# Optimization experiments

Hardware: AMD Instinct MI355X
Metric: run time of the kernel (lower is better)

Reference implementation:

```python
import jax, jax.numpy as jnp
import numpy as np

L = 2          # num_bigbird_encoder_blocks
H = 8          # n_heads
BS = 64        # block_size
G = 2          # num_global_blocks
W = 3          # window_size (blocks)
EPS = 1e-8


def rmsnorm(x, w, eps=EPS):
    return x * jax.lax.rsqrt(jnp.mean(x * x, axis=-1, keepdims=True) + eps) * w


def setup_inputs() -> dict:
    key = jax.random.key(0)
    ks = jax.random.split(key, 12)
    B, S, D, F, V = 8, 2048, 256, 1024, 32000
    nB = S // BS
    inp = {
        "input_ids": jax.random.randint(ks[0], (B, S), 0, V, dtype=jnp.int64),
        "rand_idx": jax.random.randint(ks[1], (nB, 2), 0, nB, dtype=jnp.int32),
        "emb": jax.random.normal(ks[2], (V, D), jnp.float32) * 0.02,
        "ln1_w": jnp.ones((L, D), jnp.float32),
        "wq": jax.random.normal(ks[3], (L, D, D), jnp.float32) / np.sqrt(D),
        "wk": jax.random.normal(ks[4], (L, D, D), jnp.float32) / np.sqrt(D),
        "wv": jax.random.normal(ks[5], (L, D, D), jnp.float32) / np.sqrt(D),
        "wo": jax.random.normal(ks[6], (L, D, D), jnp.float32) / np.sqrt(D),
        "ln2_w": jnp.ones((L, D), jnp.float32),
        "w1": jax.random.normal(ks[7], (L, D, F), jnp.float32) / np.sqrt(D),
        "w2": jax.random.normal(ks[8], (L, F, D), jnp.float32) / np.sqrt(F),
        "final_ln_w": jnp.ones((D,), jnp.float32),
    }
    return inp


def _split_heads(x, B, nB, dh):
    # [B,S,D] -> [B,H,nB,bs,dh]
    return x.reshape(B, nB, BS, H, dh).transpose(0, 3, 1, 2, 4)


def reference(input_ids, rand_idx, emb, ln1_w, wq, wk, wv, wo, ln2_w, w1, w2, final_ln_w):
    B, S = input_ids.shape
    D = emb.shape[1]
    dh = D // H
    nB = S // BS
    scale = 1.0 / np.sqrt(dh)

    # block-sparse key-block indices per query block: global + sliding window + random
    blocks = jnp.arange(nB)
    win = jnp.clip(blocks[:, None] + jnp.arange(-(W // 2), W // 2 + 1)[None, :], 0, nB - 1)
    glob = jnp.broadcast_to(jnp.arange(G), (nB, G))
    idx = jnp.concatenate([glob, win, rand_idx.astype(jnp.int32)], axis=1)  # [nB, M], M=7
    M = idx.shape[1]

    x = emb[input_ids]  # [B,S,D]
    for l in range(L):
        h = rmsnorm(x, ln1_w[l])
        q = _split_heads(h @ wq[l], B, nB, dh)  # [B,H,nB,bs,dh]
        k = _split_heads(h @ wk[l], B, nB, dh)
        v = _split_heads(h @ wv[l], B, nB, dh)
        k_sel = k[:, :, idx]  # [B,H,nB,M,bs,dh]
        v_sel = v[:, :, idx]
        scores = jnp.einsum("bhnqd,bhnmsd->bhnqms", q, k_sel) * scale
        a = jax.nn.softmax(scores.reshape(B, H, nB, BS, M * BS), axis=-1)
        a = a.reshape(B, H, nB, BS, M, BS)
        o = jnp.einsum("bhnqms,bhnmsd->bhnqd", a, v_sel)
        o = o.transpose(0, 2, 3, 1, 4).reshape(B, S, D)
        x = x + o @ wo[l]
        h2 = rmsnorm(x, ln2_w[l])
        x = x + jax.nn.gelu(h2 @ w1[l]) @ w2[l]
    return rmsnorm(x, final_ln_w)
```

## Files before the change

kernel.cpp:

```cpp
#include <hip/hip_runtime.h>
#include <cstdint>
#include <cstddef>

typedef __bf16 bf16x8 __attribute__((ext_vector_type(8)));
typedef __bf16 bf16x4 __attribute__((ext_vector_type(4)));
typedef float  f32x4  __attribute__((ext_vector_type(4)));
typedef unsigned u32x2 __attribute__((ext_vector_type(2)));
typedef unsigned u32x4 __attribute__((ext_vector_type(4)));

#define DMODEL 256

__device__ __forceinline__ float bflo(unsigned u) { return __builtin_bit_cast(float, u << 16); }
__device__ __forceinline__ float bfhi(unsigned u) { return __builtin_bit_cast(float, u & 0xffff0000u); }
__device__ __forceinline__ unsigned short bfbits(float f) {
  return __builtin_bit_cast(unsigned short, (__bf16)f);
}

#define GLOAD_LDS16(gp, lp) __builtin_amdgcn_global_load_lds(                 \
    (const __attribute__((address_space(1))) unsigned*)(gp),                  \
    (__attribute__((address_space(3))) unsigned*)(lp), 16, 0, 0)

__global__ void transpose_all(const float* __restrict__ wq, const float* __restrict__ wk,
                              const float* __restrict__ wv, const float* __restrict__ wo,
                              const float* __restrict__ w1, const float* __restrict__ w2,
                              __bf16* __restrict__ wbase) {
  int idx = blockIdx.x * 256 + threadIdx.x;
  int l = idx >= 786432;
  int r = idx - l * 786432;
  __bf16* wb = wbase + (size_t)l * 786432;
  const float* s; __bf16* d; int R, C, e;
  if (r < 65536)       { s = wq + l * 65536;  d = wb;          R = 256;  C = 256;  e = r; }
  else if (r < 131072) { s = wk + l * 65536;  d = wb + 65536;  R = 256;  C = 256;  e = r - 65536; }
  else if (r < 196608) { s = wv + l * 65536;  d = wb + 131072; R = 256;  C = 256;  e = r - 131072; }
  else if (r < 262144) { s = wo + l * 65536;  d = wb + 196608; R = 256;  C = 256;  e = r - 196608; }
  else if (r < 524288) { s = w1 + l * 262144; d = wb + 262144; R = 256;  C = 1024; e = r - 262144; }
  else                 { s = w2 + l * 262144; d = wb + 524288; R = 1024; C = 256;  e = r - 524288; }
  int row = e / C, col = e - row * C;
  d[col * R + row] = (__bf16)s[e];
}

__global__ void embed_k(const int* __restrict__ ids, const float* __restrict__ emb, float* __restrict__ x) {
  int row = blockIdx.x * 4 + (threadIdx.x >> 6);
  int lane = threadIdx.x & 63;
  int id = ids[row];
  ((f32x4*)(x + (size_t)row * DMODEL))[lane] = ((const f32x4*)(emb + (size_t)id * DMODEL))[lane];
}

template<typename OUT>
__global__ void rmsnorm_k(const float* __restrict__ x, const float* __restrict__ w, OUT* __restrict__ out) {
  int row = blockIdx.x * 4 + (threadIdx.x >> 6);
  int lane = threadIdx.x & 63;
  f32x4 v = ((const f32x4*)(x + (size_t)row * DMODEL))[lane];
  float ss = v[0]*v[0] + v[1]*v[1] + v[2]*v[2] + v[3]*v[3];
  #pragma unroll
  for (int off = 1; off < 64; off <<= 1) ss += __shfl_xor(ss, off);
  float rms = rsqrtf(ss * (1.0f / DMODEL) + 1e-8f);
  f32x4 wv = ((const f32x4*)w)[lane];
  if constexpr (sizeof(OUT) == 4) {
    f32x4 o;
    o[0] = v[0]*rms*wv[0]; o[1] = v[1]*rms*wv[1]; o[2] = v[2]*rms*wv[2]; o[3] = v[3]*rms*wv[3];
    ((f32x4*)((float*)out + (size_t)row * DMODEL))[lane] = o;
  } else {
    bf16x4 o;
    o[0] = (__bf16)(v[0]*rms*wv[0]); o[1] = (__bf16)(v[1]*rms*wv[1]);
    o[2] = (__bf16)(v[2]*rms*wv[2]); o[3] = (__bf16)(v[3]*rms*wv[3]);
    ((bf16x4*)((__bf16*)out + (size_t)row * DMODEL))[lane] = o;
  }
}

__device__ __forceinline__ float gelu_f(float v) {
  return 0.5f * v * (1.0f + tanhf(0.7978845608028654f * (v + 0.044715f * v * v * v)));
}

template<bool RES, bool GELU, bool OUTB>
__launch_bounds__(256)
__global__ void gemm_bt(const __bf16* __restrict__ A, const __bf16* __restrict__ Bt,
                        __bf16* __restrict__ outb, float* __restrict__ res,
                        int K, int N) {
  __shared__ char sm[32768];
  int tid = threadIdx.x;
  int lane = tid & 63;
  int w = tid >> 6;
  int wr = w >> 1, wc = w & 1;
  int lr = lane & 15;
  int hk = lane >> 4;
  size_t bm = (size_t)blockIdx.x * 128, bn = (size_t)blockIdx.y * 128;
  const __bf16* Ab = A + bm * (size_t)K;
  const __bf16* Bb = Bt + bn * (size_t)K;

  int u0 = w * 128 + lane;
  int r0 = u0 >> 2, c0 = u0 & 3;
  int u1 = u0 + 64;
  int r1 = u1 >> 2, c1 = u1 & 3;
  size_t ga0 = (size_t)r0 * K + c0 * 8;
  size_t ga1 = (size_t)r1 * K + c1 * 8;
  int lb0 = (w * 2) * 1024;
  int lb1 = (w * 2 + 1) * 1024;

  int nt = K >> 5;
  GLOAD_LDS16(Ab + ga0, sm + lb0);
  GLOAD_LDS16(Bb + ga0, sm + 8192 + lb0);
  GLOAD_LDS16(Ab + ga1, sm + lb1);
  GLOAD_LDS16(Bb + ga1, sm + 8192 + lb1);
  __syncthreads();

  f32x4 acc[4][4] = {};
  for (int t = 0; t < nt; ++t) {
    char* cur = sm + (t & 1) * 16384;
    if (t + 1 < nt) {
      char* nxt = sm + ((t + 1) & 1) * 16384;
      int kk = (t + 1) * 32;
      GLOAD_LDS16(Ab + ga0 + kk, nxt + lb0);
      GLOAD_LDS16(Bb + ga0 + kk, nxt + 8192 + lb0);
      GLOAD_LDS16(Ab + ga1 + kk, nxt + lb1);
      GLOAD_LDS16(Bb + ga1 + kk, nxt + 8192 + lb1);
    }
    bf16x8 av[4], bv[4];
    #pragma unroll
    for (int i = 0; i < 4; ++i)
      av[i] = *(const bf16x8*)(cur + (wr * 64 + i * 16 + lr) * 64 + hk * 16);
    #pragma unroll
    for (int i = 0; i < 4; ++i)
      bv[i] = *(const bf16x8*)(cur + 8192 + (wc * 64 + i * 16 + lr) * 64 + hk * 16);
    #pragma unroll
    for (int mi = 0; mi < 4; ++mi)
      #pragma unroll
      for (int ni = 0; ni < 4; ++ni)
        acc[mi][ni] = __builtin_amdgcn_mfma_f32_16x16x32_bf16(av[mi], bv[ni], acc[mi][ni], 0, 0, 0);
    __syncthreads();
  }

  size_t row0 = bm + wr * 64 + (hk << 2);
  size_t col0 = bn + wc * 64 + lr;
  #pragma unroll
  for (int mi = 0; mi < 4; ++mi)
    #pragma unroll
    for (int ni = 0; ni < 4; ++ni)
      #pragma unroll
      for (int j = 0; j < 4; ++j) {
        size_t row = row0 + mi * 16 + j, col = col0 + ni * 16;
        float val = acc[mi][ni][j];
        if constexpr (GELU) val = gelu_f(val);
        if constexpr (RES)  res[row * N + col] += val;
        if constexpr (OUTB) outb[row * N + col] = (__bf16)val;
      }
}

#define ATTN_LDS 28672

__launch_bounds__(256, 3)
__global__ void attn_k(const __bf16* __restrict__ qkv, const int* __restrict__ rand_idx,
                       __bf16* __restrict__ o) {
  extern __shared__ char smKV[];
  int tid = threadIdx.x;
  int lane = tid & 63;
  int w = tid >> 6;
  int q16 = lane & 15, g = lane >> 4;

  int bid = blockIdx.x;
  int b = bid >> 8;
  int hh = (bid >> 5) & 7;
  int n = bid & 31;
  int r5 = rand_idx[n * 2], r6 = rand_idx[n * 2 + 1];
  int nm1 = n > 0 ? n - 1 : 0;
  int np1 = n < 31 ? n + 1 : 31;
  size_t base = (size_t)b * 2048;

  #pragma unroll
  for (int it = 0; it < 7; ++it) {
    int chunk = it * 256 + tid;
    int r = chunk >> 2, c16 = chunk & 3;
    int m = r >> 6, si = r & 63;
    int kb = m == 0 ? 0 : m == 1 ? 1 : m == 2 ? nm1 : m == 3 ? n : m == 4 ? np1 : m == 5 ? r5 : r6;
    u32x4 d = *(const u32x4*)(qkv + (base + kb * 64 + si) * 768 + 256 + hh * 32 + c16 * 8);
    *(u32x4*)(smKV + ((chunk * 16) ^ ((r & 7) << 4))) = d;
  }

  bf16x8 qf = *(const bf16x8*)(qkv + (base + n * 64 + w * 16 + q16) * 768 + hh * 32 + g * 8);

  __syncthreads();

  f32x4 st[28];
  __builtin_amdgcn_s_setprio(1);
  #pragma unroll
  for (int t = 0; t < 28; ++t) {
    int row = 16 * t + q16;
    bf16x8 kf = *(const bf16x8*)(smKV + ((row * 64 + g * 16) ^ ((q16 & 7) << 4)));
    st[t] = __builtin_amdgcn_mfma_f32_16x16x32_bf16(kf, qf, (f32x4){0.f, 0.f, 0.f, 0.f}, 0, 0, 0);
  }
  __builtin_amdgcn_s_setprio(0);

  float m0 = st[0][0], m1 = st[0][1], m2 = st[0][2], m3 = st[0][3];
  #pragma unroll
  for (int t = 1; t < 28; ++t) {
    m0 = fmaxf(m0, st[t][0]); m1 = fmaxf(m1, st[t][1]);
    m2 = fmaxf(m2, st[t][2]); m3 = fmaxf(m3, st[t][3]);
  }
  float mx = fmaxf(fmaxf(m0, m1), fmaxf(m2, m3));
  mx = fmaxf(mx, __shfl_xor(mx, 16));
  mx = fmaxf(mx, __shfl_xor(mx, 32));
  const float SC = 0.17677669529663687f * 1.4426950408889634f;
  float mc = mx * SC;

  unsigned pk0[28], pk1[28];
  float ssum = 0.f;
  #pragma unroll
  for (int t = 0; t < 28; ++t) {
    float e0 = __builtin_amdgcn_exp2f(fmaf(st[t][0], SC, -mc));
    float e1 = __builtin_amdgcn_exp2f(fmaf(st[t][1], SC, -mc));
    float e2 = __builtin_amdgcn_exp2f(fmaf(st[t][2], SC, -mc));
    float e3 = __builtin_amdgcn_exp2f(fmaf(st[t][3], SC, -mc));
    ssum += (e0 + e1) + (e2 + e3);
    pk0[t] = (unsigned)bfbits(e0) | ((unsigned)bfbits(e1) << 16);
    pk1[t] = (unsigned)bfbits(e2) | ((unsigned)bfbits(e3) << 16);
  }
  ssum += __shfl_xor(ssum, 16);
  ssum += __shfl_xor(ssum, 32);
  float inv = 1.0f / ssum;

  unsigned vreg[4][8];
  #pragma unroll
  for (int it = 0; it < 4; ++it) {
    int item = it * 256 + tid;
    if (item < 896) {
      int dp = item & 15, ko = item >> 4;
      int s0 = ko * 8;
      int m = s0 >> 6, si = s0 & 63;
      int kb = m == 0 ? 0 : m == 1 ? 1 : m == 2 ? nm1 : m == 3 ? n : m == 4 ? np1 : m == 5 ? r5 : r6;
      const unsigned* vs = (const unsigned*)(qkv + (base + kb * 64 + si) * 768 + 512 + hh * 32) + dp;
      #pragma unroll
      for (int i = 0; i < 8; ++i) vreg[it][i] = vs[(size_t)i * 384];
    }
  }

  __syncthreads();

  #pragma unroll
  for (int it = 0; it < 4; ++it) {
    int item = it * 256 + tid;
    if (item < 896) {
      int dp = item & 15, ko = item >> 4;
      u32x4 lo4, hi4;
      #pragma unroll
      for (int wd = 0; wd < 4; ++wd) {
        unsigned a = vreg[it][2 * wd], bb = vreg[it][2 * wd + 1];
        lo4[wd] = (a & 0xffffu) | (bb << 16);
        hi4[wd] = (a >> 16) | (bb & 0xffff0000u);
      }
      unsigned swz = (unsigned)((dp & 7) << 4);
      int byte0 = (2 * dp) * 896 + ko * 16;
      *(u32x4*)(smKV + (byte0 ^ swz)) = lo4;
      *(u32x4*)(smKV + ((byte0 + 896) ^ swz)) = hi4;
    }
  }

  __syncthreads();

  int src0 = q16 + 32 * (g & 1);
  int src1 = src0 + 16;
  bool hi = (g >= 2);
  f32x4 oacc[2] = {};
  __builtin_amdgcn_s_setprio(1);
  #pragma unroll
  for (int ks = 0; ks < 14; ++ks) {
    unsigned a0 = __shfl(pk0[2 * ks], src0), b0 = __shfl(pk0[2 * ks + 1], src0);
    unsigned a1 = __shfl(pk1[2 * ks], src0), b1 = __shfl(pk1[2 * ks + 1], src0);
    unsigned a2 = __shfl(pk0[2 * ks], src1), b2 = __shfl(pk0[2 * ks + 1], src1);
    unsigned a3 = __shfl(pk1[2 * ks], src1), b3 = __shfl(pk1[2 * ks + 1], src1);
    u32x4 pw;
    pw[0] = hi ? b0 : a0; pw[1] = hi ? b1 : a1;
    pw[2] = hi ? b2 : a2; pw[3] = hi ? b3 : a3;
    bf16x8 pf = __builtin_bit_cast(bf16x8, pw);
    #pragma unroll
    for (int dt = 0; dt < 2; ++dt) {
      int d = 16 * dt + q16;
      bf16x8 vf = *(const bf16x8*)(smKV + ((d * 896 + 64 * ks + 16 * g) ^ (((d >> 1) & 7) << 4)));
      oacc[dt] = __builtin_amdgcn_mfma_f32_16x16x32_bf16(vf, pf, oacc[dt], 0, 0, 0);
    }
  }
  __builtin_amdgcn_s_setprio(0);

  size_t orow = (base + n * 64 + w * 16 + q16) * 256 + hh * 32;
  #pragma unroll
  for (int dt = 0; dt < 2; ++dt) {
    u32x2 pk;
    pk[0] = (unsigned)bfbits(oacc[dt][0] * inv) | ((unsigned)bfbits(oacc[dt][1] * inv) << 16);
    pk[1] = (unsigned)bfbits(oacc[dt][2] * inv) | ((unsigned)bfbits(oacc[dt][3] * inv) << 16);
    *(u32x2*)(o + orow + 16 * dt + 4 * g) = pk;
  }
}

extern "C" void kernel_launch(void* const* d_in, const int* in_sizes, int n_in,
                              void* d_out, int out_size, void* d_ws, size_t ws_size,
                              hipStream_t stream) {
  const int*   ids      = (const int*)d_in[0];
  const int*   rand_idx = (const int*)d_in[1];
  const float* emb      = (const float*)d_in[2];
  const float* ln1      = (const float*)d_in[3];
  const float* wq       = (const float*)d_in[4];
  const float* wk       = (const float*)d_in[5];
  const float* wv       = (const float*)d_in[6];
  const float* wo       = (const float*)d_in[7];
  const float* ln2      = (const float*)d_in[8];
  const float* w1       = (const float*)d_in[9];
  const float* w2       = (const float*)d_in[10];
  const float* fln      = (const float*)d_in[11];
  float* out = (float*)d_out;

  char* ws = (char*)d_ws;
  float*  x    = (float*)ws;
  __bf16* h    = (__bf16*)(ws + 16777216);
  __bf16* qkv  = (__bf16*)(ws + 25165824);
  __bf16* obuf = (__bf16*)(ws + 50331648);
  __bf16* g    = qkv;
  __bf16* wbase = (__bf16*)(ws + 58720256);

  transpose_all<<<6144, 256, 0, stream>>>(wq, wk, wv, wo, w1, w2, wbase);
  embed_k<<<4096, 256, 0, stream>>>(ids, emb, x);

  for (int l = 0; l < 2; ++l) {
    __bf16* qkvT = wbase + (size_t)l * 786432;
    __bf16* woT  = qkvT + 196608;
    __bf16* w1T  = woT + 65536;
    __bf16* w2T  = w1T + 262144;

    rmsnorm_k<__bf16><<<4096, 256, 0, stream>>>(x, ln1 + (size_t)l * 256, h);
    gemm_bt<false, false, true><<<dim3(128, 6), 256, 0, stream>>>(h, qkvT, qkv, nullptr, 256, 768);
    attn_k<<<2048, 256, ATTN_LDS, stream>>>(qkv, rand_idx, obuf);
    gemm_bt<true, false, false><<<dim3(128, 2), 256, 0, stream>>>(obuf, woT, nullptr, x, 256, 256);
    rmsnorm_k<__bf16><<<4096, 256, 0, stream>>>(x, ln2 + (size_t)l * 256, h);
    gemm_bt<false, true, true><<<dim3(128, 8), 256, 0, stream>>>(h, w1T, g, nullptr, 256, 1024);
    gemm_bt<true, false, false><<<dim3(128, 2), 256, 0, stream>>>(g, w2T, nullptr, x, 1024, 256);
  }

  rmsnorm_k<float><<<4096, 256, 0, stream>>>(x, fln, out);
}
```

Measured before the change: 408.5 us.

## Restructure block-sparse attention as chunked online softmax with separate V LDS

The attention kernel now loads K and transposed V into separate LDS regions up front. It replaces the full 28-tile score materialization with a 7-chunk online-softmax loop that uses a lazy rescale threshold. The block index is also remapped so that consecutive workgroups span different batches. This is meant to cut register pressure (no 56 packed probability registers and no staged V registers) and to remove the extra barrier between phases. In exchange it doubles LDS per block, drops the occupancy hint, and adds per-chunk reductions and shuffles.

```diff
diff --git a/kernel.cpp b/kernel.cpp
--- a/kernel.cpp
+++ b/kernel.cpp
@@ -146,18 +146,20 @@
       }
 }
 
-#define ATTN_LDS 28672
-
-__launch_bounds__(256, 3)
+#define ATTN_LDS 57344
+
+__launch_bounds__(256)
 __global__ void attn_k(const __bf16* __restrict__ qkv, const int* __restrict__ rand_idx,
                        __bf16* __restrict__ o) {
-  extern __shared__ char smKV[];
+  extern __shared__ char sm[];
+  char* smVt = sm + 28672;
   int tid = threadIdx.x;
   int lane = tid & 63;
   int w = tid >> 6;
   int q16 = lane & 15, g = lane >> 4;
 
-  int bid = blockIdx.x;
+  int bid0 = blockIdx.x;
+  int bid = (bid0 & 7) * 256 + (bid0 >> 3);
   int b = bid >> 8;
   int hh = (bid >> 5) & 7;
   int n = bid & 31;
@@ -173,52 +175,9 @@
     int m = r >> 6, si = r & 63;
     int kb = m == 0 ? 0 : m == 1 ? 1 : m == 2 ? nm1 : m == 3 ? n : m == 4 ? np1 : m == 5 ? r5 : r6;
     u32x4 d = *(const u32x4*)(qkv + (base + kb * 64 + si) * 768 + 256 + hh * 32 + c16 * 8);
-    *(u32x4*)(smKV + ((chunk * 16) ^ ((r & 7) << 4))) = d;
-  }
-
-  bf16x8 qf = *(const bf16x8*)(qkv + (base + n * 64 + w * 16 + q16) * 768 + hh * 32 + g * 8);
-
-  __syncthreads();
-
-  f32x4 st[28];
-  __builtin_amdgcn_s_setprio(1);
-  #pragma unroll
-  for (int t = 0; t < 28; ++t) {
-    int row = 16 * t + q16;
-    bf16x8 kf = *(const bf16x8*)(smKV + ((row * 64 + g * 16) ^ ((q16 & 7) << 4)));
-    st[t] = __builtin_amdgcn_mfma_f32_16x16x32_bf16(kf, qf, (f32x4){0.f, 0.f, 0.f, 0.f}, 0, 0, 0);
-  }
-  __builtin_amdgcn_s_setprio(0);
-
-  float m0 = st[0][0], m1 = st[0][1], m2 = st[0][2], m3 = st[0][3];
-  #pragma unroll
-  for (int t = 1; t < 28; ++t) {
-    m0 = fmaxf(m0, st[t][0]); m1 = fmaxf(m1, st[t][1]);
-    m2 = fmaxf(m2, st[t][2]); m3 = fmaxf(m3, st[t][3]);
-  }
-  float mx = fmaxf(fmaxf(m0, m1), fmaxf(m2, m3));
-  mx = fmaxf(mx, __shfl_xor(mx, 16));
-  mx = fmaxf(mx, __shfl_xor(mx, 32));
-  const float SC = 0.17677669529663687f * 1.4426950408889634f;
-  float mc = mx * SC;
-
-  unsigned pk0[28], pk1[28];
-  float ssum = 0.f;
-  #pragma unroll
-  for (int t = 0; t < 28; ++t) {
-    float e0 = __builtin_amdgcn_exp2f(fmaf(st[t][0], SC, -mc));
-    float e1 = __builtin_amdgcn_exp2f(fmaf(st[t][1], SC, -mc));
-    float e2 = __builtin_amdgcn_exp2f(fmaf(st[t][2], SC, -mc));
-    float e3 = __builtin_amdgcn_exp2f(fmaf(st[t][3], SC, -mc));
-    ssum += (e0 + e1) + (e2 + e3);
-    pk0[t] = (unsigned)bfbits(e0) | ((unsigned)bfbits(e1) << 16);
-    pk1[t] = (unsigned)bfbits(e2) | ((unsigned)bfbits(e3) << 16);
-  }
-  ssum += __shfl_xor(ssum, 16);
-  ssum += __shfl_xor(ssum, 32);
-  float inv = 1.0f / ssum;
-
-  unsigned vreg[4][8];
+    *(u32x4*)(sm + ((chunk * 16) ^ ((r & 7) << 4))) = d;
+  }
+
   #pragma unroll
   for (int it = 0; it < 4; ++it) {
     int item = it * 256 + tid;
@@ -228,58 +187,99 @@
       int m = s0 >> 6, si = s0 & 63;
       int kb = m == 0 ? 0 : m == 1 ? 1 : m == 2 ? nm1 : m == 3 ? n : m == 4 ? np1 : m == 5 ? r5 : r6;
       const unsigned* vs = (const unsigned*)(qkv + (base + kb * 64 + si) * 768 + 512 + hh * 32) + dp;
-      #pragma unroll
-      for (int i = 0; i < 8; ++i) vreg[it][i] = vs[(size_t)i * 384];
-    }
-  }
-
-  __syncthreads();
-
-  #pragma unroll
-  for (int it = 0; it < 4; ++it) {
-    int item = it * 256 + tid;
-    if (item < 896) {
-      int dp = item & 15, ko = item >> 4;
+      unsigned vr[8];
+      #pragma unroll
+      for (int i = 0; i < 8; ++i) vr[i] = vs[(size_t)i * 384];
       u32x4 lo4, hi4;
       #pragma unroll
       for (int wd = 0; wd < 4; ++wd) {
-        unsigned a = vreg[it][2 * wd], bb = vreg[it][2 * wd + 1];
+        unsigned a = vr[2 * wd], bb = vr[2 * wd + 1];
         lo4[wd] = (a & 0xffffu) | (bb << 16);
         hi4[wd] = (a >> 16) | (bb & 0xffff0000u);
       }
       unsigned swz = (unsigned)((dp & 7) << 4);
       int byte0 = (2 * dp) * 896 + ko * 16;
-      *(u32x4*)(smKV + (byte0 ^ swz)) = lo4;
-      *(u32x4*)(smKV + ((byte0 + 896) ^ swz)) = hi4;
-    }
-  }
+      *(u32x4*)(smVt + (byte0 ^ swz)) = lo4;
+      *(u32x4*)(smVt + ((byte0 + 896) ^ swz)) = hi4;
+    }
+  }
+
+  bf16x8 qf = *(const bf16x8*)(qkv + (base + n * 64 + w * 16 + q16) * 768 + hh * 32 + g * 8);
 
   __syncthreads();
 
+  const float SC  = 0.17677669529663687f * 1.4426950408889634f;
+  const float THR = 8.0f / SC;
   int src0 = q16 + 32 * (g & 1);
   int src1 = src0 + 16;
   bool hi = (g >= 2);
+  float m_run = -1e30f, mc = 0.f, ssum = 0.f;
   f32x4 oacc[2] = {};
-  __builtin_amdgcn_s_setprio(1);
-  #pragma unroll
-  for (int ks = 0; ks < 14; ++ks) {
-    unsigned a0 = __shfl(pk0[2 * ks], src0), b0 = __shfl(pk0[2 * ks + 1], src0);
-    unsigned a1 = __shfl(pk1[2 * ks], src0), b1 = __shfl(pk1[2 * ks + 1], src0);
-    unsigned a2 = __shfl(pk0[2 * ks], src1), b2 = __shfl(pk0[2 * ks + 1], src1);
-    unsigned a3 = __shfl(pk1[2 * ks], src1), b3 = __shfl(pk1[2 * ks + 1], src1);
-    u32x4 pw;
-    pw[0] = hi ? b0 : a0; pw[1] = hi ? b1 : a1;
-    pw[2] = hi ? b2 : a2; pw[3] = hi ? b3 : a3;
-    bf16x8 pf = __builtin_bit_cast(bf16x8, pw);
-    #pragma unroll
-    for (int dt = 0; dt < 2; ++dt) {
-      int d = 16 * dt + q16;
-      bf16x8 vf = *(const bf16x8*)(smKV + ((d * 896 + 64 * ks + 16 * g) ^ (((d >> 1) & 7) << 4)));
-      oacc[dt] = __builtin_amdgcn_mfma_f32_16x16x32_bf16(vf, pf, oacc[dt], 0, 0, 0);
-    }
-  }
-  __builtin_amdgcn_s_setprio(0);
-
+  bool first = true;
+
+  #pragma unroll
+  for (int c = 0; c < 7; ++c) {
+    f32x4 st[4];
+    #pragma unroll
+    for (int tl = 0; tl < 4; ++tl) {
+      int row = 16 * (4 * c + tl) + q16;
+      bf16x8 kf = *(const bf16x8*)(sm + ((row * 64 + g * 16) ^ ((q16 & 7) << 4)));
+      st[tl] = __builtin_amdgcn_mfma_f32_16x16x32_bf16(kf, qf, (f32x4){0.f, 0.f, 0.f, 0.f}, 0, 0, 0);
+    }
+    float lm = st[0][0];
+    #pragma unroll
+    for (int tl = 0; tl < 4; ++tl) {
+      lm = fmaxf(lm, fmaxf(fmaxf(st[tl][0], st[tl][1]), fmaxf(st[tl][2], st[tl][3])));
+    }
+    lm = fmaxf(lm, __shfl_xor(lm, 16));
+    lm = fmaxf(lm, __shfl_xor(lm, 32));
+    if (first || !__all(lm <= m_run + THR)) {
+      float nm = fmaxf(m_run, lm);
+      float sf = __builtin_amdgcn_exp2f((m_run - nm) * SC);
+      ssum *= sf;
+      #pragma unroll
+      for (int dt = 0; dt < 2; ++dt)
+        #pragma unroll
+        for (int j = 0; j < 4; ++j) oacc[dt][j] *= sf;
+      m_run = nm;
+      mc = nm * SC;
+      first = false;
+    }
+    unsigned pk0[4], pk1[4];
+    #pragma unroll
+    for (int tl = 0; tl < 4; ++tl) {
+      float e0 = __builtin_amdgcn_exp2f(fmaf(st[tl][0], SC, -mc));
+      float e1 = __builtin_amdgcn_exp2f(fmaf(st[tl][1], SC, -mc));
+      float e2 = __builtin_amdgcn_exp2f(fmaf(st[tl][2], SC, -mc));
+      float e3 = __builtin_amdgcn_exp2f(fmaf(st[tl][3], SC, -mc));
+      ssum += (e0 + e1) + (e2 + e3);
+      pk0[tl] = (unsigned)bfbits(e0) | ((unsigned)bfbits(e1) << 16);
+      pk1[tl] = (unsigned)bfbits(e2) | ((unsigned)bfbits(e3) << 16);
+    }
+    #pragma unroll
+    for (int ksl = 0; ksl < 2; ++ksl) {
+      int ks = 2 * c + ksl;
+      int lt0 = 2 * ksl, lt1 = 2 * ksl + 1;
+      unsigned a0 = __shfl(pk0[lt0], src0), b0 = __shfl(pk0[lt1], src0);
+      unsigned a1 = __shfl(pk1[lt0], src0), b1 = __shfl(pk1[lt1], src0);
+      unsigned a2 = __shfl(pk0[lt0], src1), b2 = __shfl(pk0[lt1], src1);
+      unsigned a3 = __shfl(pk1[lt0], src1), b3 = __shfl(pk1[lt1], src1);
+      u32x4 pw;
+      pw[0] = hi ? b0 : a0; pw[1] = hi ? b1 : a1;
+      pw[2] = hi ? b2 : a2; pw[3] = hi ? b3 : a3;
+      bf16x8 pf = __builtin_bit_cast(bf16x8, pw);
+      #pragma unroll
+      for (int dt = 0; dt < 2; ++dt) {
+        int d = 16 * dt + q16;
+        bf16x8 vf = *(const bf16x8*)(smVt + ((d * 896 + 64 * ks + 16 * g) ^ (((d >> 1) & 7) << 4)));
+        oacc[dt] = __builtin_amdgcn_mfma_f32_16x16x32_bf16(vf, pf, oacc[dt], 0, 0, 0);
+      }
+    }
+  }
+
+  ssum += __shfl_xor(ssum, 16);
+  ssum += __shfl_xor(ssum, 32);
+  float inv = 1.0f / ssum;
   size_t orow = (base + n * 64 + w * 16 + q16) * 256 + hh * 32;
   #pragma unroll
   for (int dt = 0; dt < 2; ++dt) {
```

Result: faster. 400.2 us (-2.0%).
